# Optimization experiments

Measured on AMD Instinct MI355X. Metric: run time of the kernel, lower is better.

The kernel has to match this reference:

```python
import jax, jax.numpy as jnp
import numpy as np

N_SLOTS = 100000
D_IN = 256
D_OUT = 256
NUM_HOPS = 3


def setup_inputs() -> dict:
    key = jax.random.key(0)
    k1, k2, k3, k4, k5 = jax.random.split(key, 5)
    memory = jax.random.normal(k1, (N_SLOTS, D_IN), dtype=jnp.float32)
    query = jax.random.normal(k2, (1, D_IN), dtype=jnp.float32)
    # original init: uniform(0, 1) of shape [output_dim, input_dim]
    A = jax.random.uniform(k3, (D_OUT, D_IN), dtype=jnp.float32)
    B = jax.random.uniform(k4, (D_OUT, D_IN), dtype=jnp.float32)
    C = jax.random.uniform(k5, (D_OUT, D_IN), dtype=jnp.float32)
    return {"memory": memory, "query": query, "A": A, "B": B, "C": C}


def reference(memory, query, A, B, C):
    # Embed memory with A (addressing) and C (content), query with B.
    mem_m = memory @ A.T          # [n_slots, d_out]
    mem_c = memory @ C.T          # [n_slots, d_out]
    u = query @ B.T               # [1, d_out]
    for _ in range(NUM_HOPS):
        scores = (mem_m @ u.T).reshape(1, N_SLOTS)   # [1, n_slots]
        p = jax.nn.softmax(scores, axis=-1)          # attention over slots
        o = (p @ mem_c).reshape(1, D_OUT)            # weighted content sum
        u = o + u                                    # hop residual update
    return u
```

## Files before the change

### kernel.cpp

```cpp
#include <hip/hip_runtime.h>
#include <math.h>

#define D 256
#define NB 512
#define PASS_THREADS 512
#define PASS_WAVES (PASS_THREADS / 64)

__device__ __forceinline__ float wave_reduce_sum(float s) {
    s += __shfl_xor(s, 32);
    s += __shfl_xor(s, 16);
    s += __shfl_xor(s, 8);
    s += __shfl_xor(s, 4);
    s += __shfl_xor(s, 2);
    s += __shfl_xor(s, 1);
    return s;
}

__device__ __forceinline__ float wave_reduce_max(float s) {
    s = fmaxf(s, __shfl_xor(s, 32));
    s = fmaxf(s, __shfl_xor(s, 16));
    s = fmaxf(s, __shfl_xor(s, 8));
    s = fmaxf(s, __shfl_xor(s, 4));
    s = fmaxf(s, __shfl_xor(s, 2));
    s = fmaxf(s, __shfl_xor(s, 1));
    return s;
}

__global__ __launch_bounds__(1024) void mr_init(const float* __restrict__ q,
                                                const float* __restrict__ Bm,
                                                const float* __restrict__ Am,
                                                float* __restrict__ u,
                                                float* __restrict__ v) {
    __shared__ __align__(16) float sq[D];
    __shared__ float su[D];
    __shared__ float part[4][D];
    const int tid = threadIdx.x;

    if (tid < D) sq[tid] = q[tid];
    __syncthreads();

    {
        const int j = tid >> 2, qd = tid & 3;
        const float4* Br = (const float4*)(Bm + (size_t)j * D + qd * 64);
        const float4* qr = (const float4*)(sq + qd * 64);
        float acc = 0.f;
#pragma unroll
        for (int i = 0; i < 16; ++i) {
            float4 b4 = Br[i];
            float4 q4 = qr[i];
            acc += b4.x * q4.x + b4.y * q4.y + b4.z * q4.z + b4.w * q4.w;
        }
        part[qd][j] = acc;
    }
    __syncthreads();
    if (tid < D) {
        float uu = part[0][tid] + part[1][tid] + part[2][tid] + part[3][tid];
        u[tid] = uu;
        su[tid] = uu;
    }
    __syncthreads();

    {
        const int k = tid & (D - 1), h = tid >> 8;
        const int j0 = h * 64;
        float acc = 0.f;
#pragma unroll 8
        for (int jj = 0; jj < 64; ++jj)
            acc += Am[(size_t)(j0 + jj) * D + k] * su[j0 + jj];
        part[h][k] = acc;
    }
    __syncthreads();
    if (tid < D)
        v[tid] = part[0][tid] + part[1][tid] + part[2][tid] + part[3][tid];
}

__device__ __forceinline__ void online_update(float s, const float4& x,
                                              float& m, float& Z, float4& w) {
    if (s > m) {
        float r = __expf(m - s);
        Z = Z * r + 1.f;
        w.x = w.x * r + x.x;
        w.y = w.y * r + x.y;
        w.z = w.z * r + x.z;
        w.w = w.w * r + x.w;
        m = s;
    } else {
        float e = __expf(s - m);
        Z += e;
        w.x += e * x.x;
        w.y += e * x.y;
        w.z += e * x.z;
        w.w += e * x.w;
    }
}

__global__ __launch_bounds__(PASS_THREADS) void mr_pass(
        const float* __restrict__ mem, const float* __restrict__ v,
        float* __restrict__ wsM, float* __restrict__ wsZ,
        float* __restrict__ wsW, int nslots, int nwaves) {
    const int lane = threadIdx.x & 63;
    const int wid  = threadIdx.x >> 6;
    const int gwave = blockIdx.x * PASS_WAVES + wid;
    const int stride = nwaves;

    const float4 vv = ((const float4*)v)[lane];

    float  m = -INFINITY;
    float  Z = 0.f;
    float4 w = {0.f, 0.f, 0.f, 0.f};

    int slot = gwave;
    for (; slot + 3 * stride < nslots; slot += 4 * stride) {
        float4 x0 = ((const float4*)(mem + (size_t)slot * D))[lane];
        float4 x1 = ((const float4*)(mem + (size_t)(slot + stride) * D))[lane];
        float4 x2 = ((const float4*)(mem + (size_t)(slot + 2 * stride) * D))[lane];
        float4 x3 = ((const float4*)(mem + (size_t)(slot + 3 * stride) * D))[lane];
        float s0 = x0.x * vv.x + x0.y * vv.y + x0.z * vv.z + x0.w * vv.w;
        float s1 = x1.x * vv.x + x1.y * vv.y + x1.z * vv.z + x1.w * vv.w;
        float s2 = x2.x * vv.x + x2.y * vv.y + x2.z * vv.z + x2.w * vv.w;
        float s3 = x3.x * vv.x + x3.y * vv.y + x3.z * vv.z + x3.w * vv.w;
        s0 = wave_reduce_sum(s0);
        s1 = wave_reduce_sum(s1);
        s2 = wave_reduce_sum(s2);
        s3 = wave_reduce_sum(s3);
        online_update(s0, x0, m, Z, w);
        online_update(s1, x1, m, Z, w);
        online_update(s2, x2, m, Z, w);
        online_update(s3, x3, m, Z, w);
    }
    for (; slot < nslots; slot += stride) {
        float4 x = ((const float4*)(mem + (size_t)slot * D))[lane];
        float s = x.x * vv.x + x.y * vv.y + x.z * vv.z + x.w * vv.w;
        s = wave_reduce_sum(s);
        online_update(s, x, m, Z, w);
    }

    __shared__ float lm[PASS_WAVES];
    __shared__ float lz[PASS_WAVES];
    __shared__ __align__(16) float lw[PASS_WAVES][D];
    if (lane == 0) { lm[wid] = m; lz[wid] = Z; }
    *(float4*)&lw[wid][lane * 4] = w;
    __syncthreads();

    const int tid = threadIdx.x;
    if (tid < D) {
        float M = lm[0];
#pragma unroll
        for (int wq = 1; wq < PASS_WAVES; ++wq) M = fmaxf(M, lm[wq]);
        float wacc = 0.f, zacc = 0.f;
#pragma unroll
        for (int wq = 0; wq < PASS_WAVES; ++wq) {
            float fq = __expf(lm[wq] - M);
            wacc += lw[wq][tid] * fq;
            zacc += lz[wq] * fq;
        }
        wsW[(size_t)blockIdx.x * D + tid] = wacc;
        if (tid == 0) {
            wsM[blockIdx.x] = M;
            wsZ[blockIdx.x] = zacc;
        }
    }
}

__global__ __launch_bounds__(1024) void mr_combine(
        const float* __restrict__ wsM, const float* __restrict__ wsZ,
        const float* __restrict__ wsW, const float* __restrict__ Cm,
        const float* __restrict__ Am, float* __restrict__ u,
        float* __restrict__ v, float* __restrict__ out, int nb, int last) {
    __shared__ float f[NB];
    __shared__ float red[16];
    __shared__ float sMZ[2];
    __shared__ float part[4][D];
    __shared__ __align__(16) float sw[D];
    __shared__ float su[D];
    const int tid = threadIdx.x;
    const int lane = tid & 63, wv = tid >> 6;

    float lm = -INFINITY;
    for (int b = tid; b < nb; b += 1024) lm = fmaxf(lm, wsM[b]);
    lm = wave_reduce_max(lm);
    if (lane == 0) red[wv] = lm;
    __syncthreads();
    if (tid == 0) {
        float M = red[0];
#pragma unroll
        for (int i = 1; i < 16; ++i) M = fmaxf(M, red[i]);
        sMZ[0] = M;
    }
    __syncthreads();
    const float M = sMZ[0];

    float zp = 0.f;
    for (int b = tid; b < nb; b += 1024) {
        float fb = __expf(wsM[b] - M);
        f[b] = fb;
        zp += wsZ[b] * fb;
    }
    zp = wave_reduce_sum(zp);
    if (lane == 0) red[wv] = zp;
    __syncthreads();
    if (tid == 0) {
        float Z = 0.f;
#pragma unroll
        for (int i = 0; i < 16; ++i) Z += red[i];
        sMZ[1] = Z;
    }
    __syncthreads();
    const float Z = sMZ[1];

    {
        const int c = tid & (D - 1);
        const int chunk = tid >> 8;
        const int bpc = nb >> 2;
        const int b0 = chunk * bpc;
        const int b1 = b0 + bpc;
        float acc = 0.f;
#pragma unroll 8
        for (int b = b0; b < b1; ++b)
            acc += wsW[(size_t)b * D + c] * f[b];
        part[chunk][c] = acc;
    }
    __syncthreads();
    if (tid < D)
        sw[tid] = (part[0][tid] + part[1][tid] + part[2][tid] + part[3][tid]) / Z;
    __syncthreads();

    {
        const int j = tid >> 2, qd = tid & 3;
        const float4* Cr = (const float4*)(Cm + (size_t)j * D + qd * 64);
        const float4* wr = (const float4*)(sw + qd * 64);
        float acc = 0.f;
#pragma unroll
        for (int i = 0; i < 16; ++i) {
            float4 c4 = Cr[i];
            float4 w4 = wr[i];
            acc += c4.x * w4.x + c4.y * w4.y + c4.z * w4.z + c4.w * w4.w;
        }
        part[qd][j] = acc;
    }
    __syncthreads();
    if (tid < D) {
        float o = part[0][tid] + part[1][tid] + part[2][tid] + part[3][tid];
        float un = u[tid] + o;
        u[tid] = un;
        su[tid] = un;
        if (last) out[tid] = un;
    }
    __syncthreads();

    if (!last) {
        const int k = tid & (D - 1), h = tid >> 8;
        const int j0 = h * 64;
        float acc = 0.f;
#pragma unroll 8
        for (int jj = 0; jj < 64; ++jj)
            acc += Am[(size_t)(j0 + jj) * D + k] * su[j0 + jj];
        part[h][k] = acc;
        __syncthreads();
        if (tid < D)
            v[tid] = part[0][tid] + part[1][tid] + part[2][tid] + part[3][tid];
    }
}

extern "C" void kernel_launch(void* const* d_in, const int* in_sizes, int n_in,
                              void* d_out, int out_size, void* d_ws, size_t ws_size,
                              hipStream_t stream) {
    const float* mem = (const float*)d_in[0];
    const float* q   = (const float*)d_in[1];
    const float* A   = (const float*)d_in[2];
    const float* B   = (const float*)d_in[3];
    const float* C   = (const float*)d_in[4];
    float* out = (float*)d_out;
    float* ws  = (float*)d_ws;

    const int nslots = in_sizes[0] / D;

    long wsf = (long)(ws_size / 4);
    int nb = NB;
    long need = 2L * D + (long)nb * (2 + D);
    if (need > wsf) {
        nb = (int)((wsf - 2L * D) / (2 + D));
        nb &= ~3;
        if (nb < 4) nb = 4;
    }

    float* u   = ws;
    float* v   = ws + D;
    float* wsM = ws + 2 * D;
    float* wsZ = wsM + nb;
    float* wsW = wsZ + nb;

    mr_init<<<1, 1024, 0, stream>>>(q, B, A, u, v);
    for (int hop = 0; hop < 3; ++hop) {
        mr_pass<<<nb, PASS_THREADS, 0, stream>>>(mem, v, wsM, wsZ, wsW,
                                                 nslots, nb * PASS_WAVES);
        mr_combine<<<1, 1024, 0, stream>>>(wsM, wsZ, wsW, C, A, u, v, out,
                                           nb, hop == 2 ? 1 : 0);
    }
}
```

Baseline: 272.2 us.

## Split each wave into four 16-lane slot groups over contiguous slabs

The pass kernel now gives each wave a contiguous slab of slots and has each 16-lane quarter-wave process its own slot, loading four float4s per lane, so eight slots are handled per iteration with only a 4-step shuffle reduction. The online-softmax update becomes branch-uniform through __any on the max change, and the per-block merge runs over 32 partial states using a precomputed scale vector. The aim is to cut shuffle and reduction overhead per slot and to raise memory-level parallelism. In exchange, register use grows with four float4 accumulators and eight float4 loads, and the wave-wide rescale runs whenever any lane's max changes.

```diff
diff --git a/kernel.cpp b/kernel.cpp
--- a/kernel.cpp
+++ b/kernel.cpp
@@ -1,10 +1,11 @@
 #include <hip/hip_runtime.h>
 #include <math.h>
+#include <float.h>
 
 #define D 256
-#define NB 512
-#define PASS_THREADS 512
-#define PASS_WAVES (PASS_THREADS / 64)
+#define NBLK 512
+#define TPB 512
+#define WPB (TPB / 64)
 
 __device__ __forceinline__ float wave_reduce_sum(float s) {
     s += __shfl_xor(s, 32);
@@ -15,7 +16,6 @@
     s += __shfl_xor(s, 1);
     return s;
 }
-
 __device__ __forceinline__ float wave_reduce_max(float s) {
     s = fmaxf(s, __shfl_xor(s, 32));
     s = fmaxf(s, __shfl_xor(s, 16));
@@ -38,7 +38,6 @@
 
     if (tid < D) sq[tid] = q[tid];
     __syncthreads();
-
     {
         const int j = tid >> 2, qd = tid & 3;
         const float4* Br = (const float4*)(Bm + (size_t)j * D + qd * 64);
@@ -59,7 +58,6 @@
         su[tid] = uu;
     }
     __syncthreads();
-
     {
         const int k = tid & (D - 1), h = tid >> 8;
         const int j0 = h * 64;
@@ -74,91 +72,133 @@
         v[tid] = part[0][tid] + part[1][tid] + part[2][tid] + part[3][tid];
 }
 
-__device__ __forceinline__ void online_update(float s, const float4& x,
-                                              float& m, float& Z, float4& w) {
-    if (s > m) {
-        float r = __expf(m - s);
-        Z = Z * r + 1.f;
-        w.x = w.x * r + x.x;
-        w.y = w.y * r + x.y;
-        w.z = w.z * r + x.z;
-        w.w = w.w * r + x.w;
-        m = s;
-    } else {
-        float e = __expf(s - m);
-        Z += e;
-        w.x += e * x.x;
-        w.y += e * x.y;
-        w.z += e * x.z;
-        w.w += e * x.w;
-    }
-}
-
-__global__ __launch_bounds__(PASS_THREADS) void mr_pass(
+__global__ __launch_bounds__(TPB) void mr_pass(
         const float* __restrict__ mem, const float* __restrict__ v,
         float* __restrict__ wsM, float* __restrict__ wsZ,
-        float* __restrict__ wsW, int nslots, int nwaves) {
-    const int lane = threadIdx.x & 63;
-    const int wid  = threadIdx.x >> 6;
-    const int gwave = blockIdx.x * PASS_WAVES + wid;
-    const int stride = nwaves;
-
-    const float4 vv = ((const float4*)v)[lane];
-
-    float  m = -INFINITY;
-    float  Z = 0.f;
-    float4 w = {0.f, 0.f, 0.f, 0.f};
-
-    int slot = gwave;
-    for (; slot + 3 * stride < nslots; slot += 4 * stride) {
-        float4 x0 = ((const float4*)(mem + (size_t)slot * D))[lane];
-        float4 x1 = ((const float4*)(mem + (size_t)(slot + stride) * D))[lane];
-        float4 x2 = ((const float4*)(mem + (size_t)(slot + 2 * stride) * D))[lane];
-        float4 x3 = ((const float4*)(mem + (size_t)(slot + 3 * stride) * D))[lane];
-        float s0 = x0.x * vv.x + x0.y * vv.y + x0.z * vv.z + x0.w * vv.w;
-        float s1 = x1.x * vv.x + x1.y * vv.y + x1.z * vv.z + x1.w * vv.w;
-        float s2 = x2.x * vv.x + x2.y * vv.y + x2.z * vv.z + x2.w * vv.w;
-        float s3 = x3.x * vv.x + x3.y * vv.y + x3.z * vv.z + x3.w * vv.w;
-        s0 = wave_reduce_sum(s0);
-        s1 = wave_reduce_sum(s1);
-        s2 = wave_reduce_sum(s2);
-        s3 = wave_reduce_sum(s3);
-        online_update(s0, x0, m, Z, w);
-        online_update(s1, x1, m, Z, w);
-        online_update(s2, x2, m, Z, w);
-        online_update(s3, x3, m, Z, w);
-    }
-    for (; slot < nslots; slot += stride) {
-        float4 x = ((const float4*)(mem + (size_t)slot * D))[lane];
-        float s = x.x * vv.x + x.y * vv.y + x.z * vv.z + x.w * vv.w;
-        s = wave_reduce_sum(s);
-        online_update(s, x, m, Z, w);
-    }
-
-    __shared__ float lm[PASS_WAVES];
-    __shared__ float lz[PASS_WAVES];
-    __shared__ __align__(16) float lw[PASS_WAVES][D];
-    if (lane == 0) { lm[wid] = m; lz[wid] = Z; }
-    *(float4*)&lw[wid][lane * 4] = w;
-    __syncthreads();
-
-    const int tid = threadIdx.x;
+        float* __restrict__ wsW, int nslots, int nwavesTotal) {
+    const int tid  = threadIdx.x;
+    const int lane = tid & 63;
+    const int wid  = tid >> 6;
+    const int l16  = lane & 15;
+    const int g    = lane >> 4;
+    const int gwave = blockIdx.x * WPB + wid;
+
+    const int slab = (nslots + nwavesTotal - 1) / nwavesTotal;
+    const int s0 = gwave * slab;
+    const int s1 = min(s0 + slab, nslots);
+
+    const float4 v0 = ((const float4*)v)[l16];
+    const float4 v1 = ((const float4*)v)[l16 + 16];
+    const float4 v2 = ((const float4*)v)[l16 + 32];
+    const float4 v3 = ((const float4*)v)[l16 + 48];
+
+    float m = -FLT_MAX, Z = 0.f;
+    float4 w0 = {0,0,0,0}, w1 = {0,0,0,0}, w2 = {0,0,0,0}, w3 = {0,0,0,0};
+
+    for (int base = s0; base < s1; base += 8) {
+        const int slotA = base + g;
+        const int slotB = base + 4 + g;
+        const bool vA = slotA < s1;
+        const bool vB = slotB < s1;
+        const int cA = vA ? slotA : s0;
+        const int cB = vB ? slotB : s0;
+        const float4* rA = (const float4*)(mem + (size_t)cA * D);
+        const float4* rB = (const float4*)(mem + (size_t)cB * D);
+        float4 a0 = rA[l16], a1 = rA[l16 + 16], a2 = rA[l16 + 32], a3 = rA[l16 + 48];
+        float4 b0 = rB[l16], b1 = rB[l16 + 16], b2 = rB[l16 + 32], b3 = rB[l16 + 48];
+
+        float pA = a0.x*v0.x + a0.y*v0.y + a0.z*v0.z + a0.w*v0.w
+                 + a1.x*v1.x + a1.y*v1.y + a1.z*v1.z + a1.w*v1.w
+                 + a2.x*v2.x + a2.y*v2.y + a2.z*v2.z + a2.w*v2.w
+                 + a3.x*v3.x + a3.y*v3.y + a3.z*v3.z + a3.w*v3.w;
+        float pB = b0.x*v0.x + b0.y*v0.y + b0.z*v0.z + b0.w*v0.w
+                 + b1.x*v1.x + b1.y*v1.y + b1.z*v1.z + b1.w*v1.w
+                 + b2.x*v2.x + b2.y*v2.y + b2.z*v2.z + b2.w*v2.w
+                 + b3.x*v3.x + b3.y*v3.y + b3.z*v3.z + b3.w*v3.w;
+        pA += __shfl_xor(pA, 1);  pB += __shfl_xor(pB, 1);
+        pA += __shfl_xor(pA, 2);  pB += __shfl_xor(pB, 2);
+        pA += __shfl_xor(pA, 4);  pB += __shfl_xor(pB, 4);
+        pA += __shfl_xor(pA, 8);  pB += __shfl_xor(pB, 8);
+
+        {
+            float sv = vA ? pA : -FLT_MAX;
+            float mn = fmaxf(m, sv);
+            float e  = vA ? __expf(sv - mn) : 0.f;
+            if (__any(mn > m)) {
+                float sc = __expf(m - mn);
+                Z = Z * sc + e;
+                w0.x = w0.x*sc + e*a0.x; w0.y = w0.y*sc + e*a0.y; w0.z = w0.z*sc + e*a0.z; w0.w = w0.w*sc + e*a0.w;
+                w1.x = w1.x*sc + e*a1.x; w1.y = w1.y*sc + e*a1.y; w1.z = w1.z*sc + e*a1.z; w1.w = w1.w*sc + e*a1.w;
+                w2.x = w2.x*sc + e*a2.x; w2.y = w2.y*sc + e*a2.y; w2.z = w2.z*sc + e*a2.z; w2.w = w2.w*sc + e*a2.w;
+                w3.x = w3.x*sc + e*a3.x; w3.y = w3.y*sc + e*a3.y; w3.z = w3.z*sc + e*a3.z; w3.w = w3.w*sc + e*a3.w;
+                m = mn;
+            } else {
+                Z += e;
+                w0.x += e*a0.x; w0.y += e*a0.y; w0.z += e*a0.z; w0.w += e*a0.w;
+                w1.x += e*a1.x; w1.y += e*a1.y; w1.z += e*a1.z; w1.w += e*a1.w;
+                w2.x += e*a2.x; w2.y += e*a2.y; w2.z += e*a2.z; w2.w += e*a2.w;
+                w3.x += e*a3.x; w3.y += e*a3.y; w3.z += e*a3.z; w3.w += e*a3.w;
+            }
+        }
+        {
+            float sv = vB ? pB : -FLT_MAX;
+            float mn = fmaxf(m, sv);
+            float e  = vB ? __expf(sv - mn) : 0.f;
+            if (__any(mn > m)) {
+                float sc = __expf(m - mn);
+                Z = Z * sc + e;
+                w0.x = w0.x*sc + e*b0.x; w0.y = w0.y*sc + e*b0.y; w0.z = w0.z*sc + e*b0.z; w0.w = w0.w*sc + e*b0.w;
+                w1.x = w1.x*sc + e*b1.x; w1.y = w1.y*sc + e*b1.y; w1.z = w1.z*sc + e*b1.z; w1.w = w1.w*sc + e*b1.w;
+                w2.x = w2.x*sc + e*b2.x; w2.y = w2.y*sc + e*b2.y; w2.z = w2.z*sc + e*b2.z; w2.w = w2.w*sc + e*b2.w;
+                w3.x = w3.x*sc + e*b3.x; w3.y = w3.y*sc + e*b3.y; w3.z = w3.z*sc + e*b3.z; w3.w = w3.w*sc + e*b3.w;
+                m = mn;
+            } else {
+                Z += e;
+                w0.x += e*b0.x; w0.y += e*b0.y; w0.z += e*b0.z; w0.w += e*b0.w;
+                w1.x += e*b1.x; w1.y += e*b1.y; w1.z += e*b1.z; w1.w += e*b1.w;
+                w2.x += e*b2.x; w2.y += e*b2.y; w2.z += e*b2.z; w2.w += e*b2.w;
+                w3.x += e*b3.x; w3.y += e*b3.y; w3.z += e*b3.z; w3.w += e*b3.w;
+            }
+        }
+    }
+
+    __shared__ __align__(16) float lw[WPB * 4][D];
+    __shared__ float lm[WPB * 4];
+    __shared__ float lz[WPB * 4];
+    __shared__ float lf[WPB * 4];
+    const int grp = wid * 4 + g;
+    *(float4*)&lw[grp][(l16 +  0) * 4] = w0;
+    *(float4*)&lw[grp][(l16 + 16) * 4] = w1;
+    *(float4*)&lw[grp][(l16 + 32) * 4] = w2;
+    *(float4*)&lw[grp][(l16 + 48) * 4] = w3;
+    if (l16 == 0) { lm[grp] = m; lz[grp] = Z; }
+    __syncthreads();
+
+    if (tid < 32) {
+        float mm = lm[tid];
+        float M = mm;
+        M = fmaxf(M, __shfl_xor(M, 1));
+        M = fmaxf(M, __shfl_xor(M, 2));
+        M = fmaxf(M, __shfl_xor(M, 4));
+        M = fmaxf(M, __shfl_xor(M, 8));
+        M = fmaxf(M, __shfl_xor(M, 16));
+        float fv = __expf(mm - M);
+        lf[tid] = fv;
+        float zf = lz[tid] * fv;
+        zf += __shfl_xor(zf, 1);
+        zf += __shfl_xor(zf, 2);
+        zf += __shfl_xor(zf, 4);
+        zf += __shfl_xor(zf, 8);
+        zf += __shfl_xor(zf, 16);
+        if (tid == 0) { wsM[blockIdx.x] = M; wsZ[blockIdx.x] = zf; }
+    }
+    __syncthreads();
+
     if (tid < D) {
-        float M = lm[0];
-#pragma unroll
-        for (int wq = 1; wq < PASS_WAVES; ++wq) M = fmaxf(M, lm[wq]);
-        float wacc = 0.f, zacc = 0.f;
-#pragma unroll
-        for (int wq = 0; wq < PASS_WAVES; ++wq) {
-            float fq = __expf(lm[wq] - M);
-            wacc += lw[wq][tid] * fq;
-            zacc += lz[wq] * fq;
-        }
+        float wacc = 0.f;
+#pragma unroll
+        for (int p = 0; p < WPB * 4; ++p) wacc += lw[p][tid] * lf[p];
         wsW[(size_t)blockIdx.x * D + tid] = wacc;
-        if (tid == 0) {
-            wsM[blockIdx.x] = M;
-            wsZ[blockIdx.x] = zacc;
-        }
     }
 }
 
@@ -167,7 +207,7 @@
         const float* __restrict__ wsW, const float* __restrict__ Cm,
         const float* __restrict__ Am, float* __restrict__ u,
         float* __restrict__ v, float* __restrict__ out, int nb, int last) {
-    __shared__ float f[NB];
+    __shared__ float f[NBLK];
     __shared__ float red[16];
     __shared__ float sMZ[2];
     __shared__ float part[4][D];
@@ -176,7 +216,7 @@
     const int tid = threadIdx.x;
     const int lane = tid & 63, wv = tid >> 6;
 
-    float lm = -INFINITY;
+    float lm = -FLT_MAX;
     for (int b = tid; b < nb; b += 1024) lm = fmaxf(lm, wsM[b]);
     lm = wave_reduce_max(lm);
     if (lane == 0) red[wv] = lm;
@@ -212,8 +252,7 @@
         const int c = tid & (D - 1);
         const int chunk = tid >> 8;
         const int bpc = nb >> 2;
-        const int b0 = chunk * bpc;
-        const int b1 = b0 + bpc;
+        const int b0 = chunk * bpc, b1 = b0 + bpc;
         float acc = 0.f;
 #pragma unroll 8
         for (int b = b0; b < b1; ++b)
@@ -276,7 +315,7 @@
     const int nslots = in_sizes[0] / D;
 
     long wsf = (long)(ws_size / 4);
-    int nb = NB;
+    int nb = NBLK;
     long need = 2L * D + (long)nb * (2 + D);
     if (need > wsf) {
         nb = (int)((wsf - 2L * D) / (2 + D));
@@ -292,8 +331,8 @@
 
     mr_init<<<1, 1024, 0, stream>>>(q, B, A, u, v);
     for (int hop = 0; hop < 3; ++hop) {
-        mr_pass<<<nb, PASS_THREADS, 0, stream>>>(mem, v, wsM, wsZ, wsW,
-                                                 nslots, nb * PASS_WAVES);
+        mr_pass<<<nb, TPB, 0, stream>>>(mem, v, wsM, wsZ, wsW,
+                                        nslots, nb * WPB);
         mr_combine<<<1, 1024, 0, stream>>>(wsM, wsZ, wsW, C, A, u, v, out,
                                            nb, hop == 2 ? 1 : 0);
     }
```

Measured after the change: 275.1 us. About the same (+1.0%).
